# Kernel optimization log

Hardware: AMD Instinct MI355X
Metric: run time of the kernel (lower is better)

The kernel has to match this reference:

```python
import jax, jax.numpy as jnp
import numpy as np

TRANSLATE_STD = 0.125
SCALE_STD = 0.2
CUTOUT_SIZE = 0.5

B, C, H, W = 64, 3, 512, 512


def setup_inputs() -> dict:
    key = jax.random.key(0)
    ks = jax.random.split(key, 20)
    inp = {
        'images': jax.random.normal(ks[0], (B, C, H, W), dtype=jnp.float32),
        'u_angle': jax.random.uniform(ks[1], (B,), dtype=jnp.float32),
        'u_scale': jax.random.uniform(ks[2], (B,), dtype=jnp.float32),
        'u_trans': jax.random.uniform(ks[3], (B,), dtype=jnp.float32),
        'u_bright': jax.random.uniform(ks[4], (B,), dtype=jnp.float32),
        'u_contrast': jax.random.uniform(ks[5], (B,), dtype=jnp.float32),
        'u_sat': jax.random.uniform(ks[6], (B,), dtype=jnp.float32),
        'noise': jax.random.normal(ks[7], (B, C, H, W), dtype=jnp.float32),
        'm_flip': jax.random.randint(ks[8], (B,), 0, 2, dtype=jnp.int32),
        'm_rot': jax.random.randint(ks[9], (B,), 0, 2, dtype=jnp.int32),
        'm_scale': jax.random.randint(ks[10], (B,), 0, 2, dtype=jnp.int32),
        'm_trans': jax.random.randint(ks[11], (B,), 0, 2, dtype=jnp.int32),
        'm_bright': jax.random.randint(ks[12], (B,), 0, 2, dtype=jnp.int32),
        'm_contrast': jax.random.randint(ks[13], (B,), 0, 2, dtype=jnp.int32),
        'm_sat': jax.random.randint(ks[14], (B,), 0, 2, dtype=jnp.int32),
        'm_cut': jax.random.randint(ks[15], (B,), 0, 2, dtype=jnp.int32),
        'y0': jax.random.randint(ks[16], (B,), 0, H - int(H * CUTOUT_SIZE) + 1, dtype=jnp.int32),
        'x0': jax.random.randint(ks[17], (B,), 0, W - int(W * CUTOUT_SIZE) + 1, dtype=jnp.int32),
    }
    return inp


def _sample_bilinear_reflect(img, gx, gy):
    # img: [C,H,W]; gx, gy: [H,W] normalized coords in grid_sample convention
    # (align_corners=False, padding_mode='reflection')
    c, h, w = img.shape
    x = ((gx + 1.0) * w - 1.0) * 0.5
    y = ((gy + 1.0) * h - 1.0) * 0.5

    def reflect(v, size):
        # reflect about pixel edges [-0.5, size-0.5], then clip coordinate
        v = jnp.abs(v + 0.5)
        v = jnp.mod(v, 2.0 * size)
        v = jnp.minimum(v, 2.0 * size - v)
        return jnp.clip(v - 0.5, 0.0, size - 1.0)

    x = reflect(x, float(w))
    y = reflect(y, float(h))
    x0f = jnp.floor(x)
    y0f = jnp.floor(y)
    wx = x - x0f
    wy = y - y0f
    x0i = jnp.clip(x0f, 0, w - 1).astype(jnp.int32)
    x1i = jnp.clip(x0f + 1, 0, w - 1).astype(jnp.int32)
    y0i = jnp.clip(y0f, 0, h - 1).astype(jnp.int32)
    y1i = jnp.clip(y0f + 1, 0, h - 1).astype(jnp.int32)
    v00 = img[:, y0i, x0i]
    v01 = img[:, y0i, x1i]
    v10 = img[:, y1i, x0i]
    v11 = img[:, y1i, x1i]
    top = v00 + wx * (v01 - v00)
    bot = v10 + wx * (v11 - v10)
    return top + wy * (bot - top)


def reference(images, u_angle, u_scale, u_trans, u_bright, u_contrast, u_sat,
              noise, m_flip, m_rot, m_scale, m_trans, m_bright, m_contrast,
              m_sat, m_cut, y0, x0):
    b, c, h, w = images.shape
    # xflip
    images = jnp.where((m_flip > 0)[:, None, None, None], images[..., ::-1], images)
    # rotate / scale / translate (single value broadcast to both axes, as in original)
    angle = jnp.where(m_rot > 0, (u_angle * 2.0 - 1.0) * jnp.pi, 0.0)
    sc = jnp.where(m_scale > 0, (u_scale * 2.0 - 1.0) * SCALE_STD + 1.0, 1.0)
    tr = jnp.where(m_trans > 0, (u_trans * 2.0 - 1.0) * TRANSLATE_STD, 0.0)
    ca = jnp.cos(angle)[:, None, None]
    sa = jnp.sin(angle)[:, None, None]
    scb = sc[:, None, None]
    trb = tr[:, None, None]
    gx0, gy0 = jnp.meshgrid(jnp.linspace(-1.0, 1.0, w), jnp.linspace(-1.0, 1.0, h), indexing='xy')  # [H,W]
    gx = scb * (ca * gx0 - sa * gy0) + trb  # [B,H,W]
    gy = scb * (sa * gx0 + ca * gy0) + trb
    images = jax.vmap(_sample_bilinear_reflect)(images, gx, gy)
    # brightness
    bb = jnp.where(m_bright > 0, u_bright * 0.2, 0.0)
    images = jnp.clip(images + bb[:, None, None, None], -1.0, 1.0)
    # contrast
    cc = jnp.where(m_contrast > 0, u_contrast + 0.5, 1.0)
    images = jnp.clip(images * cc[:, None, None, None], -1.0, 1.0)
    # saturation: lerp(grayscale, images, s)
    ss = jnp.where(m_sat > 0, u_sat * 2.0, 1.0)[:, None, None, None]
    gray = images.mean(axis=1, keepdims=True)
    images = jnp.clip(gray + ss * (images - gray), -1.0, 1.0)
    ch, cw = int(h * CUTOUT_SIZE), int(w * CUTOUT_SIZE)
    ys = jnp.arange(h)[None, :, None]
    xs = jnp.arange(w)[None, None, :]
    y0b = y0[:, None, None]
    x0b = x0[:, None, None]
    cmask = (ys >= y0b) & (ys < y0b + ch) & (xs >= x0b) & (xs < x0b + cw)
    fmask = cmask & (m_cut > 0)[:, None, None]
    images = jnp.where(fmask[:, None, :, :], noise, images)
    return images
```

## Files before the change

kernel.cpp:

```cpp
#include <hip/hip_runtime.h>
#include <math.h>


constexpr int Bn = 64;
constexpr int Cn = 3;
constexpr int Hn = 512;
constexpr int Wn = 512;
constexpr float TRANSLATE_STD = 0.125f;
constexpr float SCALE_STD = 0.2f;
constexpr int CUT_H = 256;
constexpr int CUT_W = 256;

__device__ __forceinline__ float reflect_coord(float v, float size) {
    v = fabsf(v + 0.5f);
    v = fmodf(v, 2.0f * size);
    v = fminf(v, 2.0f * size - v);
    return fminf(fmaxf(v - 0.5f, 0.0f), size - 1.0f);
}

__global__ __launch_bounds__(256) void augment_kernel(
    const float* __restrict__ images,
    const float* __restrict__ u_angle,
    const float* __restrict__ u_scale,
    const float* __restrict__ u_trans,
    const float* __restrict__ u_bright,
    const float* __restrict__ u_contrast,
    const float* __restrict__ u_sat,
    const float* __restrict__ noise,
    const int* __restrict__ m_flip,
    const int* __restrict__ m_rot,
    const int* __restrict__ m_scale,
    const int* __restrict__ m_trans,
    const int* __restrict__ m_bright,
    const int* __restrict__ m_contrast,
    const int* __restrict__ m_sat,
    const int* __restrict__ m_cut,
    const int* __restrict__ y0p,
    const int* __restrict__ x0p,
    float* __restrict__ out)
{
    const int x = blockIdx.x * 256 + threadIdx.x;
    const int y = blockIdx.y;
    const int b = blockIdx.z;

    const float angle = (m_rot[b] > 0) ? (u_angle[b] * 2.0f - 1.0f) * 3.14159265358979323846f : 0.0f;
    const float sc    = (m_scale[b] > 0) ? (u_scale[b] * 2.0f - 1.0f) * SCALE_STD + 1.0f : 1.0f;
    const float tr    = (m_trans[b] > 0) ? (u_trans[b] * 2.0f - 1.0f) * TRANSLATE_STD : 0.0f;
    const float bb    = (m_bright[b] > 0) ? u_bright[b] * 0.2f : 0.0f;
    const float cc    = (m_contrast[b] > 0) ? u_contrast[b] + 0.5f : 1.0f;
    const float ss    = (m_sat[b] > 0) ? u_sat[b] * 2.0f : 1.0f;
    const bool  flip  = m_flip[b] > 0;
    const bool  docut = m_cut[b] > 0;
    const int   cy0   = y0p[b];
    const int   cx0   = x0p[b];

    float saf, caf;
    __sincosf(angle, &saf, &caf);

    const float gx0 = -1.0f + (2.0f / 511.0f) * (float)x;
    const float gy0 = -1.0f + (2.0f / 511.0f) * (float)y;

    const float gx = sc * (caf * gx0 - saf * gy0) + tr;
    const float gy = sc * (saf * gx0 + caf * gy0) + tr;

    float xx = ((gx + 1.0f) * (float)Wn - 1.0f) * 0.5f;
    float yy = ((gy + 1.0f) * (float)Hn - 1.0f) * 0.5f;
    xx = reflect_coord(xx, (float)Wn);
    yy = reflect_coord(yy, (float)Hn);

    const float x0f = floorf(xx);
    const float y0f = floorf(yy);
    const float wx = xx - x0f;
    const float wy = yy - y0f;

    int x0i = (int)fminf(fmaxf(x0f, 0.0f), (float)(Wn - 1));
    int x1i = (int)fminf(x0f + 1.0f, (float)(Wn - 1));
    int y0i = (int)fminf(fmaxf(y0f, 0.0f), (float)(Hn - 1));
    int y1i = (int)fminf(y0f + 1.0f, (float)(Hn - 1));

    if (flip) { x0i = (Wn - 1) - x0i; x1i = (Wn - 1) - x1i; }

    const size_t plane = (size_t)Hn * Wn;
    const float* imgb = images + (size_t)b * Cn * plane;
    const int r0 = y0i * Wn;
    const int r1 = y1i * Wn;

    float vals[Cn];
    #pragma unroll
    for (int c = 0; c < Cn; ++c) {
        const float* p = imgb + (size_t)c * plane;
        const float v00 = p[r0 + x0i];
        const float v01 = p[r0 + x1i];
        const float v10 = p[r1 + x0i];
        const float v11 = p[r1 + x1i];
        const float top = v00 + wx * (v01 - v00);
        const float bot = v10 + wx * (v11 - v10);
        float v = top + wy * (bot - top);
        v = fminf(fmaxf(v + bb, -1.0f), 1.0f);
        v = fminf(fmaxf(v * cc, -1.0f), 1.0f);
        vals[c] = v;
    }

    const float gray = (vals[0] + vals[1] + vals[2]) * (1.0f / 3.0f);
    const bool cut = docut && (y >= cy0) && (y < cy0 + CUT_H) && (x >= cx0) && (x < cx0 + CUT_W);

    const size_t base = (size_t)b * Cn * plane + (size_t)y * Wn + (size_t)x;
    #pragma unroll
    for (int c = 0; c < Cn; ++c) {
        float v = gray + ss * (vals[c] - gray);
        v = fminf(fmaxf(v, -1.0f), 1.0f);
        if (cut) v = noise[base + c * plane];
        out[base + c * plane] = v;
    }
}

extern "C" void kernel_launch(void* const* d_in, const int* in_sizes, int n_in,
                              void* d_out, int out_size, void* d_ws, size_t ws_size,
                              hipStream_t stream) {
    const float* images     = (const float*)d_in[0];
    const float* u_angle    = (const float*)d_in[1];
    const float* u_scale    = (const float*)d_in[2];
    const float* u_trans    = (const float*)d_in[3];
    const float* u_bright   = (const float*)d_in[4];
    const float* u_contrast = (const float*)d_in[5];
    const float* u_sat      = (const float*)d_in[6];
    const float* noise      = (const float*)d_in[7];
    const int*   m_flip     = (const int*)d_in[8];
    const int*   m_rot      = (const int*)d_in[9];
    const int*   m_scale    = (const int*)d_in[10];
    const int*   m_trans    = (const int*)d_in[11];
    const int*   m_bright   = (const int*)d_in[12];
    const int*   m_contrast = (const int*)d_in[13];
    const int*   m_sat      = (const int*)d_in[14];
    const int*   m_cut      = (const int*)d_in[15];
    const int*   y0p        = (const int*)d_in[16];
    const int*   x0p        = (const int*)d_in[17];
    float* out = (float*)d_out;

    dim3 block(256);
    dim3 grid(Wn / 256, Hn, Bn);
    augment_kernel<<<grid, block, 0, stream>>>(
        images, u_angle, u_scale, u_trans, u_bright, u_contrast, u_sat, noise,
        m_flip, m_rot, m_scale, m_trans, m_bright, m_contrast, m_sat, m_cut,
        y0p, x0p, out);
}
```

Before: 587.6 us.

## Use 2D 32x8 thread tiles, paired 8-byte gathers, and nontemporal stores

Changes the block shape from a 256-wide row strip to a 32x8 2D tile, so rotated sampling footprints stay local in cache. It replaces the four scalar bilinear gathers per channel with two 8-byte vector loads per row, picking each tap with a select. It also marks the noise loads and the output stores as nontemporal so they do not evict the image data being sampled. The 8-byte loads may be misaligned when the x offset is odd, which could add cost on some addresses.

```diff
diff --git a/kernel.cpp b/kernel.cpp
--- a/kernel.cpp
+++ b/kernel.cpp
@@ -10,6 +10,14 @@
 constexpr float SCALE_STD = 0.2f;
 constexpr int CUT_H = 256;
 constexpr int CUT_W = 256;
+
+typedef float f2v __attribute__((ext_vector_type(2)));
+
+__device__ __forceinline__ f2v load2(const float* p) {
+    f2v r;
+    __builtin_memcpy(&r, p, 8);
+    return r;
+}
 
 __device__ __forceinline__ float reflect_coord(float v, float size) {
     v = fabsf(v + 0.5f);
@@ -39,8 +47,8 @@
     const int* __restrict__ x0p,
     float* __restrict__ out)
 {
-    const int x = blockIdx.x * 256 + threadIdx.x;
-    const int y = blockIdx.y;
+    const int x = blockIdx.x * 32 + threadIdx.x;
+    const int y = blockIdx.y * 8 + threadIdx.y;
     const int b = blockIdx.z;
 
     const float angle = (m_rot[b] > 0) ? (u_angle[b] * 2.0f - 1.0f) * 3.14159265358979323846f : 0.0f;
@@ -75,24 +83,30 @@
 
     int x0i = (int)fminf(fmaxf(x0f, 0.0f), (float)(Wn - 1));
     int x1i = (int)fminf(x0f + 1.0f, (float)(Wn - 1));
-    int y0i = (int)fminf(fmaxf(y0f, 0.0f), (float)(Hn - 1));
-    int y1i = (int)fminf(y0f + 1.0f, (float)(Hn - 1));
+    const int y0i = (int)fminf(fmaxf(y0f, 0.0f), (float)(Hn - 1));
+    const int y1i = (int)fminf(y0f + 1.0f, (float)(Hn - 1));
 
     if (flip) { x0i = (Wn - 1) - x0i; x1i = (Wn - 1) - x1i; }
 
+    const int xbase = min(min(x0i, x1i), Wn - 2);
+    const bool s0 = (x0i != xbase);
+    const bool s1 = (x1i != xbase);
+
     const size_t plane = (size_t)Hn * Wn;
     const float* imgb = images + (size_t)b * Cn * plane;
-    const int r0 = y0i * Wn;
-    const int r1 = y1i * Wn;
+    const int r0 = y0i * Wn + xbase;
+    const int r1 = y1i * Wn + xbase;
 
     float vals[Cn];
     #pragma unroll
     for (int c = 0; c < Cn; ++c) {
         const float* p = imgb + (size_t)c * plane;
-        const float v00 = p[r0 + x0i];
-        const float v01 = p[r0 + x1i];
-        const float v10 = p[r1 + x0i];
-        const float v11 = p[r1 + x1i];
+        const f2v t0 = load2(p + r0);
+        const f2v t1 = load2(p + r1);
+        const float v00 = s0 ? t0.y : t0.x;
+        const float v01 = s1 ? t0.y : t0.x;
+        const float v10 = s0 ? t1.y : t1.x;
+        const float v11 = s1 ? t1.y : t1.x;
         const float top = v00 + wx * (v01 - v00);
         const float bot = v10 + wx * (v11 - v10);
         float v = top + wy * (bot - top);
@@ -109,8 +123,8 @@
     for (int c = 0; c < Cn; ++c) {
         float v = gray + ss * (vals[c] - gray);
         v = fminf(fmaxf(v, -1.0f), 1.0f);
-        if (cut) v = noise[base + c * plane];
-        out[base + c * plane] = v;
+        if (cut) v = __builtin_nontemporal_load(&noise[base + c * plane]);
+        __builtin_nontemporal_store(v, &out[base + c * plane]);
     }
 }
 
@@ -137,8 +151,8 @@
     const int*   x0p        = (const int*)d_in[17];
     float* out = (float*)d_out;
 
-    dim3 block(256);
-    dim3 grid(Wn / 256, Hn, Bn);
+    dim3 block(32, 8);
+    dim3 grid(Wn / 32, Hn / 8, Bn);
     augment_kernel<<<grid, block, 0, stream>>>(
         images, u_angle, u_scale, u_trans, u_bright, u_contrast, u_sat, noise,
         m_flip, m_rot, m_scale, m_trans, m_bright, m_contrast, m_sat, m_cut,
```

New measurement: 511.5 us. 1.15x faster.
